# Performance work log

Hardware: AMD Instinct MI355X
Metric: run time of the kernel (lower is better)

The kernel has to match this reference:

```python
import jax, jax.numpy as jnp
import numpy as np

N = 50000
E = 800000
HID = 128
EDGE_D = 1
NORM_FACTOR = 100.0


def setup_inputs() -> dict:
    key = jax.random.key(0)
    ks = jax.random.split(key, 12)
    in_dim = 2 * HID + EDGE_D  # 257
    # Xavier-uniform-ish init scales
    def xavier(k, shape, gain=1.0):
        fan_in, fan_out = shape[0], shape[1]
        a = gain * np.sqrt(6.0 / (fan_in + fan_out))
        return jax.random.uniform(k, shape, jnp.float32, -a, a)
    return {
        "h": jax.random.normal(ks[0], (N, HID), jnp.float32),
        "coord": jax.random.normal(ks[1], (N, 3), jnp.float32),
        "coord_diff": jax.random.normal(ks[2], (E, 3), jnp.float32),
        "coord_cross": jax.random.normal(ks[3], (E, 3), jnp.float32),
        "edge_attr": jax.random.normal(ks[4], (E, EDGE_D), jnp.float32),
        "edge_index": jax.random.randint(ks[5], (2, E), 0, N, jnp.int64),
        "W1": xavier(ks[6], (in_dim, HID)),
        "b1": jnp.zeros((HID,), jnp.float32),
        "W2": xavier(ks[7], (HID, HID)),
        "b2": jnp.zeros((HID,), jnp.float32),
        "W3": xavier(ks[8], (HID, 1), gain=0.001),
    }


def reference(h, coord, coord_diff, coord_cross, edge_attr, edge_index, W1, b1, W2, b2, W3):
    # reflection_equiv=True, tanh=False -> coord_cross unused, no tanh clamp
    row, col = edge_index[0], edge_index[1]
    # gather endpoint features and concat with edge attributes: [E, 2*HID+1]
    inp = jnp.concatenate([h[row], h[col], edge_attr], axis=1)
    x = jax.nn.silu(inp @ W1 + b1)
    x = jax.nn.silu(x @ W2 + b2)
    phi = x @ W3                      # [E, 1]
    trans = coord_diff * phi          # [E, 3]
    # unsorted_segment_sum over row with 'sum' aggregation (divide by norm factor)
    agg = jax.ops.segment_sum(trans, row, num_segments=coord.shape[0]) / NORM_FACTOR
    return coord + agg
```

## Files before the change

### kernel.cpp

```cpp
#include <hip/hip_runtime.h>
#include <stdint.h>

#define N_NODES 50000
#define E_EDGES 800000
#define HID 128
#define NGROUP 25000
#define BE 128
#define XS_STRIDE 264
#define YS_STRIDE 136
#define HS_STRIDE 132
#define CS_STRIDE 132

typedef unsigned short u16;
typedef unsigned char u8;
typedef __attribute__((ext_vector_type(8))) short svec8;
typedef __attribute__((ext_vector_type(16))) float fvec16;
typedef __attribute__((ext_vector_type(4))) unsigned uvec4;
typedef __attribute__((ext_vector_type(2))) unsigned uvec2;
typedef __attribute__((ext_vector_type(2))) float fvec2;

union frag_u { uvec4 u; svec8 s; };

__device__ __forceinline__ float bf2f(u16 u) {
    union { unsigned int i; float f; } v; v.i = ((unsigned int)u) << 16; return v.f;
}
__device__ __forceinline__ u16 f2bf(float f) {
    union { float f; unsigned int i; } v; v.f = f;
    unsigned int u = v.i;
    return (u16)((u + 0x7fffu + ((u >> 16) & 1u)) >> 16);
}
__device__ __forceinline__ unsigned f2u(float f) {
    union { float f; unsigned i; } v; v.f = f; return v.i;
}
__device__ __forceinline__ float lo16(unsigned u) {
    union { unsigned i; float f; } v; v.i = u << 16; return v.f;
}
__device__ __forceinline__ float hi16(unsigned u) {
    union { unsigned i; float f; } v; v.i = u & 0xFFFF0000u; return v.f;
}
__device__ __forceinline__ float silu_f(float x) {
    return x * __builtin_amdgcn_rcpf(1.0f + __expf(-x));
}
__device__ __forceinline__ float ldf(const void* p, size_t i, int is_bf) {
    return is_bf ? bf2f(((const u16*)p)[i]) : ((const float*)p)[i];
}
__device__ __forceinline__ int ldi(const void* p, size_t i, int is_i64) {
    return is_i64 ? ((const int*)p)[2 * i] : ((const int*)p)[i];
}

__device__ __forceinline__ void gld_lds16(const void* g, void* l) {
    __builtin_amdgcn_global_load_lds(
        (const __attribute__((address_space(1))) unsigned*)g,
        (__attribute__((address_space(3))) unsigned*)l, 16, 0, 0);
}

__device__ __forceinline__ int detect_bf_w(const void* p) {
    unsigned u = ((const u16*)p)[2 * (threadIdx.x & 63)];
    unsigned e = (u >> 7) & 0xFFu;
    unsigned long long m = __ballot(e >= 100u && e <= 140u);
    return __popcll(m) >= 48;
}
__device__ __forceinline__ int detect_i64_w(const void* eidx) {
    unsigned long long m = __ballot(((const int*)eidx)[2 * (threadIdx.x & 63) + 1] == 0);
    return __popcll(m) >= 48;
}

__global__ void transpose_w(const void* __restrict__ W1, const void* __restrict__ W2,
                            u16* __restrict__ W1t, u16* __restrict__ W2t,
                            u16* __restrict__ w1lb, float* __restrict__ agg) {
    const int is_bf = detect_bf_w(W1);
    int n = blockIdx.x;
    int k = threadIdx.x;
    W1t[n * 256 + k] = f2bf(ldf(W1, (size_t)k * 128 + n, is_bf));
    if (k < 128) W2t[n * 128 + k] = f2bf(ldf(W2, (size_t)k * 128 + n, is_bf));
    if (n == 0 && k < 128) w1lb[k] = f2bf(ldf(W1, (size_t)256 * 128 + k, is_bf));
    for (int i = blockIdx.x * 256 + k; i < N_NODES * 3; i += 128 * 256) agg[i] = 0.0f;
}

__global__ __launch_bounds__(256) void precompute_p(
    const void* __restrict__ h, const void* __restrict__ b1,
    const u16* __restrict__ W1t, u8* __restrict__ P)
{
    __shared__ __align__(16) union SMem {
        u16 Hs[128 * HS_STRIDE];
        float Cs[128 * CS_STRIDE];
    } sm;
    const int tid = threadIdx.x;
    const int is_bf = detect_bf_w(h);
    const int base = blockIdx.x * 128;
    {
        const int rr = tid >> 5, c = tid & 31;
        for (int it = 0; it < 16; ++it) {
            int row = it * 8 + rr;
            int node = base + row; if (node > N_NODES - 1) node = N_NODES - 1;
            u16* dst = &sm.Hs[row * HS_STRIDE + c * 4];
            if (is_bf) {
                *(uint2*)dst = *(const uint2*)((const u16*)h + (size_t)node * HID + c * 4);
            } else {
                float4 v = *(const float4*)((const float*)h + (size_t)node * HID + c * 4);
                uint2 w;
                w.x = (unsigned)f2bf(v.x) | ((unsigned)f2bf(v.y) << 16);
                w.y = (unsigned)f2bf(v.z) | ((unsigned)f2bf(v.w) << 16);
                *(uint2*)dst = w;
            }
        }
    }
    __syncthreads();
    const int lane = tid & 63, wv = tid >> 6, l31 = lane & 31, hi = lane >> 5;
    fvec16 acc[8] = {};
    for (int ks = 0; ks < 8; ++ks) {
        const int kk = ks * 16 + hi * 8;
        svec8 af = *(const svec8*)(&sm.Hs[(wv * 32 + l31) * HS_STRIDE + kk]);
        #pragma unroll
        for (int t = 0; t < 8; ++t) {
            const int n = t * 32 + l31;
            const u16* bp = (t < 4) ? (W1t + n * 256 + kk)
                                    : (W1t + (n - 128) * 256 + 128 + kk);
            svec8 bf = *(const svec8*)bp;
            acc[t] = __builtin_amdgcn_mfma_f32_32x32x16_bf16(af, bf, acc[t], 0, 0, 0);
        }
    }
    __syncthreads();
    #pragma unroll
    for (int half = 0; half < 2; ++half) {
        #pragma unroll
        for (int t = 0; t < 4; ++t) {
            const int tt = half * 4 + t;
            const int n = t * 32 + l31;
            const float bias = (half == 0) ? ldf(b1, n, is_bf) : 0.0f;
            #pragma unroll
            for (int r = 0; r < 16; ++r) {
                int m = (r & 3) + 8 * (r >> 2) + 4 * hi;
                sm.Cs[(wv * 32 + m) * CS_STRIDE + n] = acc[tt][r] + bias;
            }
        }
        __syncthreads();
        #pragma unroll
        for (int i = 0; i < 4; ++i) {
            int row = i * 32 + (tid >> 3);
            int node = base + row;
            if (node < N_NODES) {
                const float* src = &sm.Cs[row * CS_STRIDE + (tid & 7) * 16];
                uvec4 outv;
                #pragma unroll
                for (int d = 0; d < 4; ++d) {
                    int w = __builtin_amdgcn_cvt_pk_fp8_f32(src[d * 4 + 0], src[d * 4 + 1], 0, false);
                    w     = __builtin_amdgcn_cvt_pk_fp8_f32(src[d * 4 + 2], src[d * 4 + 3], w, true);
                    outv[d] = (unsigned)w;
                }
                *(uvec4*)(P + (size_t)node * 256 + half * 128 + (tid & 7) * 16) = outv;
            }
        }
        __syncthreads();
    }
}

__global__ __launch_bounds__(256, 2) void egnn_edge_p(
    const u8* __restrict__ P, const void* __restrict__ coord_diff,
    const void* __restrict__ edge_attr, const void* __restrict__ edge_index,
    const u16* __restrict__ w1lb, const void* __restrict__ b2,
    const void* __restrict__ W3, const u16* __restrict__ W2t,
    float* __restrict__ agg)
{
    __shared__ __align__(16) u16 W2f[16384];
    __shared__ __align__(16) u8  PB[4][8192];
    __shared__ __align__(16) u16 w1ls[128];
    const int tid = threadIdx.x;
    #pragma unroll
    for (int i = 0; i < 8; ++i) {
        int f = i * 256 + tid;
        int t = f >> 9, ks = (f >> 6) & 7, fh = (f >> 5) & 1, fl = f & 31;
        *(svec8*)(&W2f[f * 8]) = *(const svec8*)(W2t + (t * 32 + fl) * 128 + fh * 64 + ks * 8);
    }
    if (tid < 16) *(uvec4*)(&w1ls[tid * 8]) = *(const uvec4*)(w1lb + tid * 8);
    const int is_bf = detect_bf_w(edge_attr);
    const int is_i64 = detect_i64_w(edge_index);
    const int lane = tid & 63, wv = tid >> 6, l31 = lane & 31, hi = lane >> 5;

    float b2c[4], w3c[4];
    #pragma unroll
    for (int t = 0; t < 4; ++t) {
        int c = t * 32 + l31;
        b2c[t] = ldf(b2, c, is_bf);
        w3c[t] = ldf(W3, c, is_bf);
    }
    __syncthreads();

    u8* const pbw = &PB[wv][0];

    const int b0 = l31 & 1, bb1 = (l31 >> 1) & 1, bb2 = (l31 >> 2) & 1, bb3 = (l31 >> 3) & 1;
    const int rr = (b0 << 3) | (bb1 << 2) | (bb2 << 1) | bb3;
    const int em = (rr & 3) + 8 * (rr >> 2) + 4 * hi;

    const int wid = blockIdx.x * 4 + wv, nw = gridDim.x * 4;
    int g = wid;
    int rowN = 0, colN = 0; float eaN = 0.0f, ea_cur = 0.0f;
    {
        const int e = g * 32 + l31;
        const int row0 = ldi(edge_index, (size_t)e, is_i64);
        const int col0 = ldi(edge_index, (size_t)E_EDGES + e, is_i64);
        ea_cur = ldf(edge_attr, (size_t)e, is_bf);
        const u8* pr = P + (size_t)row0 * 256 + hi * 64;
        const u8* pc = P + (size_t)col0 * 256 + 128 + hi * 64;
        __builtin_amdgcn_sched_barrier(0);
        #pragma unroll
        for (int j = 0; j < 4; ++j) gld_lds16(pr + j * 16, pbw + j * 1024);
        #pragma unroll
        for (int j = 0; j < 4; ++j) gld_lds16(pc + j * 16, pbw + 4096 + j * 1024);
        __builtin_amdgcn_sched_barrier(0);
        const int gn = g + nw;
        const int en = gn * 32 + l31;
        rowN = ldi(edge_index, (size_t)en, is_i64);
        colN = ldi(edge_index, (size_t)E_EDGES + en, is_i64);
        eaN  = ldf(edge_attr, (size_t)en, is_bf);
    }
    while (g < NGROUP) {
        const int gn = g + nw;
        asm volatile("s_waitcnt vmcnt(3)" ::: "memory");
        uvec4 pv1[4], pv2[4];
        #pragma unroll
        for (int j = 0; j < 4; ++j) pv1[j] = *(const uvec4*)(pbw + j * 1024 + lane * 16);
        #pragma unroll
        for (int j = 0; j < 4; ++j) pv2[j] = *(const uvec4*)(pbw + 4096 + j * 1024 + lane * 16);
        frag_u af[8];
        #pragma unroll
        for (int ks = 0; ks < 8; ++ks) {
            const unsigned a0 = pv1[ks >> 1][(ks & 1) * 2];
            const unsigned a1 = pv1[ks >> 1][(ks & 1) * 2 + 1];
            const unsigned c0 = pv2[ks >> 1][(ks & 1) * 2];
            const unsigned c1 = pv2[ks >> 1][(ks & 1) * 2 + 1];
            float q1[8], q2[8];
            {
                fvec2 t0 = __builtin_amdgcn_cvt_pk_f32_fp8((int)a0, false);
                fvec2 t1 = __builtin_amdgcn_cvt_pk_f32_fp8((int)a0, true);
                fvec2 t2 = __builtin_amdgcn_cvt_pk_f32_fp8((int)a1, false);
                fvec2 t3 = __builtin_amdgcn_cvt_pk_f32_fp8((int)a1, true);
                q1[0] = t0[0]; q1[1] = t0[1]; q1[2] = t1[0]; q1[3] = t1[1];
                q1[4] = t2[0]; q1[5] = t2[1]; q1[6] = t3[0]; q1[7] = t3[1];
                fvec2 s0 = __builtin_amdgcn_cvt_pk_f32_fp8((int)c0, false);
                fvec2 s1 = __builtin_amdgcn_cvt_pk_f32_fp8((int)c0, true);
                fvec2 s2 = __builtin_amdgcn_cvt_pk_f32_fp8((int)c1, false);
                fvec2 s3 = __builtin_amdgcn_cvt_pk_f32_fp8((int)c1, true);
                q2[0] = s0[0]; q2[1] = s0[1]; q2[2] = s1[0]; q2[3] = s1[1];
                q2[4] = s2[0]; q2[5] = s2[1]; q2[6] = s3[0]; q2[7] = s3[1];
            }
            const uvec4 wl = *(const uvec4*)(&w1ls[(hi * 8 + ks) * 8]);
            #pragma unroll
            for (int p = 0; p < 4; ++p) {
                const unsigned uw = wl[p];
                float xl = q1[2 * p]     + q2[2 * p]     + ea_cur * lo16(uw);
                float xh = q1[2 * p + 1] + q2[2 * p + 1] + ea_cur * hi16(uw);
                float yl = silu_f(xl), yh = silu_f(xh);
                af[ks].u[p] = (f2u(yl) >> 16) | (f2u(yh) & 0xFFFF0000u);
            }
        }
        int rowN2 = 0, colN2 = 0; float eaN2 = 0.0f;
        if (gn + nw < NGROUP) {
            const int en = (gn + nw) * 32 + l31;
            rowN2 = ldi(edge_index, (size_t)en, is_i64);
            colN2 = ldi(edge_index, (size_t)E_EDGES + en, is_i64);
            eaN2  = ldf(edge_attr, (size_t)en, is_bf);
        }
        const int eg = g * 32 + em;
        const int r2 = ldi(edge_index, (size_t)eg, is_i64);
        float cd0, cd1;
        if (l31 < 16) {
            cd0 = ldf(coord_diff, (size_t)eg * 3 + 0, is_bf);
            cd1 = ldf(coord_diff, (size_t)eg * 3 + 1, is_bf);
        } else {
            cd0 = ldf(coord_diff, (size_t)eg * 3 + 2, is_bf);
            cd1 = 0.0f;
        }
        __builtin_amdgcn_sched_barrier(0);
        if (gn < NGROUP) {
            const u8* pr = P + (size_t)rowN * 256 + hi * 64;
            const u8* pc = P + (size_t)colN * 256 + 128 + hi * 64;
            #pragma unroll
            for (int j = 0; j < 4; ++j) gld_lds16(pr + j * 16, pbw + j * 1024);
            #pragma unroll
            for (int j = 0; j < 4; ++j) gld_lds16(pc + j * 16, pbw + 4096 + j * 1024);
        }
        __builtin_amdgcn_sched_barrier(0);
        float s[16];
        #pragma unroll
        for (int r = 0; r < 16; ++r) s[r] = 0.0f;
        #pragma unroll
        for (int t = 0; t < 4; ++t) {
            fvec16 acc = {};
            #pragma unroll
            for (int ks = 0; ks < 8; ++ks) {
                svec8 bf = *(const svec8*)(&W2f[((t * 8 + ks) * 2 + hi) * 256 + l31 * 8]);
                acc = __builtin_amdgcn_mfma_f32_32x32x16_bf16(af[ks].s, bf, acc, 0, 0, 0);
            }
            #pragma unroll
            for (int r = 0; r < 16; ++r)
                s[r] += silu_f(acc[r] + b2c[t]) * w3c[t];
        }
        #pragma unroll
        for (int r = 0; r < 16; ++r) s[r] += __shfl_xor(s[r], 1);
        float w4[8];
        #pragma unroll
        for (int j = 0; j < 8; ++j) w4[j] = b0 ? s[j + 8] : s[j];
        #pragma unroll
        for (int j = 0; j < 8; ++j) w4[j] += __shfl_xor(w4[j], 2);
        float x4[4];
        #pragma unroll
        for (int j = 0; j < 4; ++j) x4[j] = bb1 ? w4[j + 4] : w4[j];
        #pragma unroll
        for (int j = 0; j < 4; ++j) x4[j] += __shfl_xor(x4[j], 4);
        float y2[2];
        y2[0] = bb2 ? x4[2] : x4[0];
        y2[1] = bb2 ? x4[3] : x4[1];
        y2[0] += __shfl_xor(y2[0], 8);
        y2[1] += __shfl_xor(y2[1], 8);
        float z = bb3 ? y2[1] : y2[0];
        z += __shfl_xor(z, 16);
        if (l31 < 16) {
            atomicAdd(&agg[r2 * 3 + 0], cd0 * z);
            atomicAdd(&agg[r2 * 3 + 1], cd1 * z);
        } else {
            atomicAdd(&agg[r2 * 3 + 2], cd0 * z);
        }
        g = gn; ea_cur = eaN;
        rowN = rowN2; colN = colN2; eaN = eaN2;
    }
}

__global__ __launch_bounds__(256, 2) void egnn_edge_kernel(
    const void* __restrict__ h, const void* __restrict__ coord_diff,
    const void* __restrict__ edge_attr, const void* __restrict__ edge_index,
    const void* __restrict__ W1, const void* __restrict__ b1,
    const void* __restrict__ b2, const void* __restrict__ W3,
    const u16* __restrict__ W1t, const u16* __restrict__ W2t,
    float* __restrict__ agg)
{
    __shared__ __align__(16) u16 Xs[BE * XS_STRIDE];
    __shared__ int   rows_s[BE];
    __shared__ int   cols_s[BE];
    __shared__ float ea_s[BE];
    __shared__ float b1_s[HID], b2_s[HID], w1l_s[HID], w3_s[HID];

    const int tid = threadIdx.x;
    const int e0  = blockIdx.x * BE;
    const int is_bf  = detect_bf_w(h);
    const int is_i64 = detect_i64_w(edge_index);

    if (tid < BE) {
        rows_s[tid] = ldi(edge_index, (size_t)(e0 + tid), is_i64);
        cols_s[tid] = ldi(edge_index, (size_t)(E_EDGES + e0 + tid), is_i64);
        ea_s[tid]   = ldf(edge_attr, (size_t)(e0 + tid), is_bf);
    }
    if (tid < HID) {
        b1_s[tid]  = ldf(b1, tid, is_bf);
        b2_s[tid]  = ldf(b2, tid, is_bf);
        w1l_s[tid] = ldf(W1, (size_t)256 * 128 + tid, is_bf);
        w3_s[tid]  = ldf(W3, tid, is_bf);
    }
    __syncthreads();
    {
        const int gg = tid >> 4, c = tid & 15;
        #pragma unroll
        for (int it = 0; it < 16; ++it) {
            int hr = it * 16 + gg;
            int e = hr >> 1, half = hr & 1;
            int src = half ? cols_s[e] : rows_s[e];
            svec8 v;
            if (is_bf) {
                v = *(const svec8*)((const u16*)h + (size_t)src * HID + c * 8);
            } else {
                const float* hf = (const float*)h + (size_t)src * HID + c * 8;
                float4 va = *(const float4*)hf;
                float4 vb = *(const float4*)(hf + 4);
                v[0] = (short)f2bf(va.x); v[1] = (short)f2bf(va.y);
                v[2] = (short)f2bf(va.z); v[3] = (short)f2bf(va.w);
                v[4] = (short)f2bf(vb.x); v[5] = (short)f2bf(vb.y);
                v[6] = (short)f2bf(vb.z); v[7] = (short)f2bf(vb.w);
            }
            *(svec8*)(&Xs[e * XS_STRIDE + half * 128 + c * 8]) = v;
        }
    }
    __syncthreads();
    const int lane = tid & 63;
    const int wv   = tid >> 6;
    const int l31  = lane & 31, hi = lane >> 5;
    const int col  = wv * 32 + l31;

    fvec16 acc[4] = {};
    for (int ks = 0; ks < 16; ++ks) {
        const int kk = ks * 16 + hi * 8;
        svec8 bfrag = *(const svec8*)(W1t + col * 256 + kk);
        #pragma unroll
        for (int mt = 0; mt < 4; ++mt) {
            svec8 afrag = *(const svec8*)(&Xs[(mt * 32 + l31) * XS_STRIDE + kk]);
            acc[mt] = __builtin_amdgcn_mfma_f32_32x32x16_bf16(afrag, bfrag, acc[mt], 0, 0, 0);
        }
    }
    __syncthreads();
    u16* Ys = Xs;
    #pragma unroll
    for (int mt = 0; mt < 4; ++mt)
        #pragma unroll
        for (int r = 0; r < 16; ++r) {
            int row = mt * 32 + (r & 3) + 8 * (r >> 2) + 4 * hi;
            float v = acc[mt][r] + ea_s[row] * w1l_s[col] + b1_s[col];
            Ys[row * YS_STRIDE + col] = f2bf(silu_f(v));
        }
    __syncthreads();
    fvec16 acc2[4] = {};
    for (int ks = 0; ks < 8; ++ks) {
        const int kk = ks * 16 + hi * 8;
        svec8 bfrag = *(const svec8*)(W2t + col * 128 + kk);
        #pragma unroll
        for (int mt = 0; mt < 4; ++mt) {
            svec8 afrag = *(const svec8*)(&Ys[(mt * 32 + l31) * YS_STRIDE + kk]);
            acc2[mt] = __builtin_amdgcn_mfma_f32_32x32x16_bf16(afrag, bfrag, acc2[mt], 0, 0, 0);
        }
    }
    __syncthreads();
    #pragma unroll
    for (int mt = 0; mt < 4; ++mt)
        #pragma unroll
        for (int r = 0; r < 16; ++r) {
            int row = mt * 32 + (r & 3) + 8 * (r >> 2) + 4 * hi;
            float v = acc2[mt][r] + b2_s[col];
            Ys[row * YS_STRIDE + col] = f2bf(silu_f(v));
        }
    __syncthreads();
    if (tid < BE) {
        const int e = tid;
        float phi = 0.0f;
        #pragma unroll
        for (int j = 0; j < 16; ++j) {
            svec8 x = *(const svec8*)(&Ys[e * YS_STRIDE + j * 8]);
            #pragma unroll
            for (int t = 0; t < 8; ++t)
                phi += bf2f((u16)x[t]) * w3_s[j * 8 + t];
        }
        const size_t ei = (size_t)(e0 + e);
        const int r = rows_s[e];
        atomicAdd(&agg[r * 3 + 0], ldf(coord_diff, ei * 3 + 0, is_bf) * phi);
        atomicAdd(&agg[r * 3 + 1], ldf(coord_diff, ei * 3 + 1, is_bf) * phi);
        atomicAdd(&agg[r * 3 + 2], ldf(coord_diff, ei * 3 + 2, is_bf) * phi);
    }
}

__global__ void finalize_kernel(const void* __restrict__ coord,
                                const float* __restrict__ agg,
                                void* __restrict__ out) {
    const int is_bf = detect_bf_w(coord);
    int i = blockIdx.x * blockDim.x + threadIdx.x;
    if (i < N_NODES * 3) {
        float v = ldf(coord, i, is_bf) + agg[i] * 0.01f;
        if (is_bf) ((u16*)out)[i] = f2bf(v);
        else       ((float*)out)[i] = v;
    }
}

extern "C" void kernel_launch(void* const* d_in, const int* in_sizes, int n_in,
                              void* d_out, int out_size, void* d_ws, size_t ws_size,
                              hipStream_t stream) {
    const void* h          = d_in[0];
    const void* coord      = d_in[1];
    const void* coord_diff = d_in[2];
    const void* edge_attr  = d_in[4];
    const void* edge_index = d_in[5];
    const void* W1 = d_in[6];
    const void* b1 = d_in[7];
    const void* W2 = d_in[8];
    const void* b2 = d_in[9];
    const void* W3 = d_in[10];

    char* ws    = (char*)d_ws;
    float* agg  = (float*)ws;
    u16* W1t    = (u16*)(ws + 600064);
    u16* W2t    = (u16*)(ws + 665600);
    u16* w1lb   = (u16*)(ws + 698432);
    u8* P       = (u8*)(ws + 698880);
    const size_t NEED = 698880 + (size_t)N_NODES * 256;

    transpose_w<<<dim3(128), dim3(256), 0, stream>>>(W1, W2, W1t, W2t, w1lb, agg);

    if (ws_size >= NEED) {
        precompute_p<<<dim3((N_NODES + 127) / 128), dim3(256), 0, stream>>>(
            h, b1, W1t, P);
        egnn_edge_p<<<dim3(512), dim3(256), 0, stream>>>(
            P, coord_diff, edge_attr, edge_index, w1lb, b2, W3, W2t, agg);
    } else {
        egnn_edge_kernel<<<dim3(E_EDGES / BE), dim3(256), 0, stream>>>(
            h, coord_diff, edge_attr, edge_index, W1, b1, b2, W3, W1t, W2t, agg);
    }
    finalize_kernel<<<dim3((N_NODES * 3 + 255) / 256), dim3(256), 0, stream>>>(coord, agg, d_out);
}
```

Before: 250.8 us.

## Use FP8 MFMA for second layer and retile node precompute

The second edge MLP layer now runs on fp8 MFMA instead of bf16. W2 is stored in shared memory as fp8 and the SiLU activations are packed into fp8 fragments. The node precompute kernel is retiled to 64 nodes per block, with the four waves split across row and column tiles to cut per-wave accumulator registers. The edge kernel grid grows from 512 to 768 blocks. This halves the shared memory for W2 and gives higher MFMA throughput, but it loses precision in a hidden layer, which may hurt accuracy.

```diff
diff --git a/kernel.cpp b/kernel.cpp
--- a/kernel.cpp
+++ b/kernel.cpp
@@ -19,8 +19,6 @@
 typedef __attribute__((ext_vector_type(2))) unsigned uvec2;
 typedef __attribute__((ext_vector_type(2))) float fvec2;
 
-union frag_u { uvec4 u; svec8 s; };
-
 __device__ __forceinline__ float bf2f(u16 u) {
     union { unsigned int i; float f; } v; v.i = ((unsigned int)u) << 16; return v.f;
 }
@@ -28,9 +26,6 @@
     union { float f; unsigned int i; } v; v.f = f;
     unsigned int u = v.i;
     return (u16)((u + 0x7fffu + ((u >> 16) & 1u)) >> 16);
-}
-__device__ __forceinline__ unsigned f2u(float f) {
-    union { float f; unsigned i; } v; v.f = f; return v.i;
 }
 __device__ __forceinline__ float lo16(unsigned u) {
     union { unsigned i; float f; } v; v.i = u << 16; return v.f;
@@ -82,15 +77,16 @@
     const u16* __restrict__ W1t, u8* __restrict__ P)
 {
     __shared__ __align__(16) union SMem {
-        u16 Hs[128 * HS_STRIDE];
-        float Cs[128 * CS_STRIDE];
+        u16 Hs[64 * HS_STRIDE];
+        float Cs[64 * CS_STRIDE];
     } sm;
     const int tid = threadIdx.x;
     const int is_bf = detect_bf_w(h);
-    const int base = blockIdx.x * 128;
+    const int base = blockIdx.x * 64;
     {
         const int rr = tid >> 5, c = tid & 31;
-        for (int it = 0; it < 16; ++it) {
+        #pragma unroll
+        for (int it = 0; it < 8; ++it) {
             int row = it * 8 + rr;
             int node = base + row; if (node > N_NODES - 1) node = N_NODES - 1;
             u16* dst = &sm.Hs[row * HS_STRIDE + c * 4];
@@ -107,36 +103,40 @@
     }
     __syncthreads();
     const int lane = tid & 63, wv = tid >> 6, l31 = lane & 31, hi = lane >> 5;
-    fvec16 acc[8] = {};
+    const int mb = (wv & 1) * 32;
+    const int tb = (wv >> 1) * 4;
+    fvec16 acc[4] = {};
     for (int ks = 0; ks < 8; ++ks) {
         const int kk = ks * 16 + hi * 8;
-        svec8 af = *(const svec8*)(&sm.Hs[(wv * 32 + l31) * HS_STRIDE + kk]);
-        #pragma unroll
-        for (int t = 0; t < 8; ++t) {
+        svec8 af = *(const svec8*)(&sm.Hs[(mb + l31) * HS_STRIDE + kk]);
+        #pragma unroll
+        for (int tt = 0; tt < 4; ++tt) {
+            const int t = tb + tt;
             const int n = t * 32 + l31;
             const u16* bp = (t < 4) ? (W1t + n * 256 + kk)
                                     : (W1t + (n - 128) * 256 + 128 + kk);
             svec8 bf = *(const svec8*)bp;
-            acc[t] = __builtin_amdgcn_mfma_f32_32x32x16_bf16(af, bf, acc[t], 0, 0, 0);
+            acc[tt] = __builtin_amdgcn_mfma_f32_32x32x16_bf16(af, bf, acc[tt], 0, 0, 0);
         }
     }
     __syncthreads();
     #pragma unroll
     for (int half = 0; half < 2; ++half) {
-        #pragma unroll
-        for (int t = 0; t < 4; ++t) {
-            const int tt = half * 4 + t;
-            const int n = t * 32 + l31;
-            const float bias = (half == 0) ? ldf(b1, n, is_bf) : 0.0f;
-            #pragma unroll
-            for (int r = 0; r < 16; ++r) {
-                int m = (r & 3) + 8 * (r >> 2) + 4 * hi;
-                sm.Cs[(wv * 32 + m) * CS_STRIDE + n] = acc[tt][r] + bias;
+        if ((wv >> 1) == half) {
+            #pragma unroll
+            for (int tt = 0; tt < 4; ++tt) {
+                const int colh = tt * 32 + l31;
+                const float bias = (half == 0) ? ldf(b1, colh, is_bf) : 0.0f;
+                #pragma unroll
+                for (int r = 0; r < 16; ++r) {
+                    int m = (r & 3) + 8 * (r >> 2) + 4 * hi;
+                    sm.Cs[(mb + m) * CS_STRIDE + colh] = acc[tt][r] + bias;
+                }
             }
         }
         __syncthreads();
         #pragma unroll
-        for (int i = 0; i < 4; ++i) {
+        for (int i = 0; i < 2; ++i) {
             int row = i * 32 + (tid >> 3);
             int node = base + row;
             if (node < N_NODES) {
@@ -162,7 +162,7 @@
     const void* __restrict__ W3, const u16* __restrict__ W2t,
     float* __restrict__ agg)
 {
-    __shared__ __align__(16) u16 W2f[16384];
+    __shared__ __align__(16) u8  W2f8[16384];
     __shared__ __align__(16) u8  PB[4][8192];
     __shared__ __align__(16) u16 w1ls[128];
     const int tid = threadIdx.x;
@@ -170,7 +170,15 @@
     for (int i = 0; i < 8; ++i) {
         int f = i * 256 + tid;
         int t = f >> 9, ks = (f >> 6) & 7, fh = (f >> 5) & 1, fl = f & 31;
-        *(svec8*)(&W2f[f * 8]) = *(const svec8*)(W2t + (t * 32 + fl) * 128 + fh * 64 + ks * 8);
+        svec8 v = *(const svec8*)(W2t + (t * 32 + fl) * 128 + fh * 64 + ks * 8);
+        float x0 = bf2f((u16)v[0]), x1 = bf2f((u16)v[1]), x2 = bf2f((u16)v[2]), x3 = bf2f((u16)v[3]);
+        float x4 = bf2f((u16)v[4]), x5 = bf2f((u16)v[5]), x6 = bf2f((u16)v[6]), x7 = bf2f((u16)v[7]);
+        int w0 = __builtin_amdgcn_cvt_pk_fp8_f32(x0, x1, 0, false);
+        w0     = __builtin_amdgcn_cvt_pk_fp8_f32(x2, x3, w0, true);
+        int w1 = __builtin_amdgcn_cvt_pk_fp8_f32(x4, x5, 0, false);
+        w1     = __builtin_amdgcn_cvt_pk_fp8_f32(x6, x7, w1, true);
+        uvec2 wv2; wv2[0] = (unsigned)w0; wv2[1] = (unsigned)w1;
+        *(uvec2*)(&W2f8[f * 8]) = wv2;
     }
     if (tid < 16) *(uvec4*)(&w1ls[tid * 8]) = *(const uvec4*)(w1lb + tid * 8);
     const int is_bf = detect_bf_w(edge_attr);
@@ -222,7 +230,7 @@
         for (int j = 0; j < 4; ++j) pv1[j] = *(const uvec4*)(pbw + j * 1024 + lane * 16);
         #pragma unroll
         for (int j = 0; j < 4; ++j) pv2[j] = *(const uvec4*)(pbw + 4096 + j * 1024 + lane * 16);
-        frag_u af[8];
+        long long af8[8];
         #pragma unroll
         for (int ks = 0; ks < 8; ++ks) {
             const unsigned a0 = pv1[ks >> 1][(ks & 1) * 2];
@@ -245,14 +253,19 @@
                 q2[4] = s2[0]; q2[5] = s2[1]; q2[6] = s3[0]; q2[7] = s3[1];
             }
             const uvec4 wl = *(const uvec4*)(&w1ls[(hi * 8 + ks) * 8]);
+            float y[8];
             #pragma unroll
             for (int p = 0; p < 4; ++p) {
                 const unsigned uw = wl[p];
                 float xl = q1[2 * p]     + q2[2 * p]     + ea_cur * lo16(uw);
                 float xh = q1[2 * p + 1] + q2[2 * p + 1] + ea_cur * hi16(uw);
-                float yl = silu_f(xl), yh = silu_f(xh);
-                af[ks].u[p] = (f2u(yl) >> 16) | (f2u(yh) & 0xFFFF0000u);
-            }
+                y[2 * p] = silu_f(xl); y[2 * p + 1] = silu_f(xh);
+            }
+            int w0 = __builtin_amdgcn_cvt_pk_fp8_f32(y[0], y[1], 0, false);
+            w0     = __builtin_amdgcn_cvt_pk_fp8_f32(y[2], y[3], w0, true);
+            int w1 = __builtin_amdgcn_cvt_pk_fp8_f32(y[4], y[5], 0, false);
+            w1     = __builtin_amdgcn_cvt_pk_fp8_f32(y[6], y[7], w1, true);
+            af8[ks] = (long long)(((unsigned long long)(unsigned)w1 << 32) | (unsigned)w0);
         }
         int rowN2 = 0, colN2 = 0; float eaN2 = 0.0f;
         if (gn + nw < NGROUP) {
@@ -289,8 +302,9 @@
             fvec16 acc = {};
             #pragma unroll
             for (int ks = 0; ks < 8; ++ks) {
-                svec8 bf = *(const svec8*)(&W2f[((t * 8 + ks) * 2 + hi) * 256 + l31 * 8]);
-                acc = __builtin_amdgcn_mfma_f32_32x32x16_bf16(af[ks].s, bf, acc, 0, 0, 0);
+                union { uvec2 u; long long l; } bu;
+                bu.u = *(const uvec2*)(&W2f8[((t * 8 + ks) * 2 + hi) * 256 + l31 * 8]);
+                acc = __builtin_amdgcn_mfma_f32_32x32x16_fp8_fp8(af8[ks], bu.l, acc, 0, 0, 0);
             }
             #pragma unroll
             for (int r = 0; r < 16; ++r)
@@ -481,9 +495,9 @@
     transpose_w<<<dim3(128), dim3(256), 0, stream>>>(W1, W2, W1t, W2t, w1lb, agg);
 
     if (ws_size >= NEED) {
-        precompute_p<<<dim3((N_NODES + 127) / 128), dim3(256), 0, stream>>>(
+        precompute_p<<<dim3((N_NODES + 63) / 64), dim3(256), 0, stream>>>(
             h, b1, W1t, P);
-        egnn_edge_p<<<dim3(512), dim3(256), 0, stream>>>(
+        egnn_edge_p<<<dim3(768), dim3(256), 0, stream>>>(
             P, coord_diff, edge_attr, edge_index, w1lb, b2, W3, W2t, agg);
     } else {
         egnn_edge_kernel<<<dim3(E_EDGES / BE), dim3(256), 0, stream>>>(
```

After: 239.0 us. -4.7%, faster.
